# Kernel optimization log

Hardware: AMD Instinct MI355X
Metric: run time of the kernel (lower is better)

## Reference

```python
import jax, jax.numpy as jnp
import numpy as np

B, R, N, D, H, QK, K = 32, 200, 200, 128, 8, 16, 10
CLIP = 10.0  # standard POMO logit clipping


def setup_inputs() -> dict:
    key = jax.random.key(0)
    ks = jax.random.split(key, 12)
    encoded_nodes = jax.random.normal(ks[0], (B, N, D), jnp.float32)
    distance = jax.random.uniform(ks[1], (B, N, N), jnp.float32)
    current = jax.random.randint(ks[2], (B, R), 0, N)
    u = jax.random.uniform(ks[3], (B, R, N))
    ninf_mask = jnp.where(u < 0.3, -jnp.inf, 0.0).astype(jnp.float32)
    s = 0.02
    Wq = jax.random.normal(ks[4], (2 * D, H * QK), jnp.float32) * s
    Wk = jax.random.normal(ks[5], (D, H * QK), jnp.float32) * s
    Wv = jax.random.normal(ks[6], (D, H * QK), jnp.float32) * s
    Wmhc = jax.random.normal(ks[7], (H * QK, D), jnp.float32) * s
    b_mhc = jnp.zeros((D,), jnp.float32)
    W1 = jax.random.normal(ks[8], (K * D, 5 * D), jnp.float32) * s
    b1 = jnp.zeros((5 * D,), jnp.float32)
    W2 = jax.random.normal(ks[9], (5 * D, D), jnp.float32) * s
    b2 = jnp.zeros((D,), jnp.float32)
    return {"encoded_nodes": encoded_nodes, "distance": distance, "ninf_mask": ninf_mask,
            "current": current, "Wq": Wq, "Wk": Wk, "Wv": Wv, "Wmhc": Wmhc, "b_mhc": b_mhc,
            "W1": W1, "b1": b1, "W2": W2, "b2": b2}


def _search_unvisited(current, distance, ninf_mask):
    # rows of distance at current nodes: [B,R,N] (avoids B*R*N*N materialization)
    dist_f = jnp.take_along_axis(distance, current[:, :, None], axis=1)
    dist_m = jnp.where(jnp.isfinite(ninf_mask), dist_f, jnp.inf)
    neg_vals, idx = jax.lax.top_k(-dist_m, K)  # k smallest distances
    vals = -neg_vals
    return jnp.where(jnp.isinf(vals), N, idx)  # pad index N for masked-out slots


def _gather_pad0(encoded_nodes, idx):
    padded = jnp.concatenate([encoded_nodes, jnp.zeros((B, 1, D), encoded_nodes.dtype)], axis=1)
    g = jnp.take_along_axis(padded, idx.reshape(B, R * K)[:, :, None], axis=1)
    return g.reshape(B, R, K, D)


def _gather_pad_avg(a):
    # replace all-zero (pad) rows by the mean of non-zero rows within each [K,D] group
    is_zero = jnp.sum(a, axis=-1) == 0  # [B,R,K]
    cnt = jnp.maximum(jnp.sum(~is_zero, axis=-1).astype(a.dtype), 1e-9)  # [B,R]
    mean = jnp.sum(a, axis=2) / cnt[..., None]  # [B,R,D]
    return jnp.where(is_zero[..., None], mean[:, :, None, :], a)


def reference(encoded_nodes, distance, ninf_mask, current,
              Wq, Wk, Wv, Wmhc, b_mhc, W1, b1, W2, b2):
    knn = _search_unvisited(current, distance, ninf_mask)         # [B,R,K]
    a = _gather_pad0(encoded_nodes, knn)                          # [B,R,K,D]
    b = _gather_pad_avg(a)                                        # [B,R,K,D]
    h = jnp.maximum(b.reshape(B, R, K * D) @ W1 + b1, 0.0)
    unv = h @ W2 + b2                                             # [B,R,D]
    cur_emb = jnp.take_along_axis(encoded_nodes, current[:, :, None], axis=1)  # [B,R,D]
    qin = jnp.concatenate([cur_emb, unv], axis=-1)                # [B,R,2D]
    q = (qin @ Wq).reshape(B, R, H, QK).transpose(0, 2, 1, 3)     # [B,H,R,QK]
    k = (encoded_nodes @ Wk).reshape(B, N, H, QK).transpose(0, 2, 1, 3)
    v = (encoded_nodes @ Wv).reshape(B, N, H, QK).transpose(0, 2, 1, 3)
    score = jnp.einsum('bhrd,bhnd->bhrn', q, k) / jnp.sqrt(jnp.float32(QK))
    score = score + ninf_mask[:, None]                            # [B,H,R,N]
    w = jax.nn.softmax(score, axis=-1)
    out = jnp.einsum('bhrn,bhnd->bhrd', w, v)
    out = out.transpose(0, 2, 1, 3).reshape(B, R, H * QK)
    mh = out @ Wmhc + b_mhc                                       # [B,R,D]
    sh = jnp.einsum('brd,bnd->brn', mh, encoded_nodes) / jnp.sqrt(jnp.float32(D))
    logits = CLIP * jnp.tanh(sh) + ninf_mask
    return jax.nn.softmax(logits, axis=-1)                        # [B,R,N]
```

## Files before the change

kernel.cpp:

```cpp
#include <hip/hip_runtime.h>
#include <hip/hip_bf16.h>
#include <math.h>

#define Bc 32
#define Rc 200
#define Nc 200
#define Dc 128
#define Hc 8
#define QKc 16
#define Kc 10
#define BRc (Bc*Rc)

typedef __attribute__((ext_vector_type(8))) short short8;
typedef __attribute__((ext_vector_type(4))) float f32x4;
typedef unsigned long long u64;

#define GLOAD_LDS16(g, l) __builtin_amdgcn_global_load_lds( \
    (const __attribute__((address_space(1))) void*)(g), \
    (__attribute__((address_space(3))) void*)(l), 16, 0, 0)

__device__ inline void transpose_tile(const float* __restrict__ src, int lds_,
                                      __hip_bfloat16* __restrict__ dst, int ldd,
                                      int k0, int n0, float scale)
{
    __shared__ float tile[32][33];
    int tx = threadIdx.x & 31, ty = threadIdx.x >> 5;
    #pragma unroll
    for (int i = ty; i < 32; i += 8)
        tile[i][tx] = src[(size_t)(k0 + i) * lds_ + n0 + tx];
    __syncthreads();
    #pragma unroll
    for (int i = ty; i < 32; i += 8)
        dst[(size_t)(n0 + i) * ldd + k0 + tx] = __float2bfloat16(tile[tx][i] * scale);
}

__global__ __launch_bounds__(256) void prep_knn_kernel(
    const float* __restrict__ W1, const float* __restrict__ W2,
    const float* __restrict__ Wq, const float* __restrict__ Wmhc,
    const float* __restrict__ Wk, const float* __restrict__ Wv,
    const float* __restrict__ b2, const float* __restrict__ enc,
    const float* __restrict__ dist, const float* __restrict__ mask,
    const int* __restrict__ cur,
    __hip_bfloat16* __restrict__ W1t, __hip_bfloat16* __restrict__ Wkvt,
    __hip_bfloat16* __restrict__ Wmb, __hip_bfloat16* __restrict__ Wcat,
    float* __restrict__ bq, __hip_bfloat16* __restrict__ encb,
    unsigned* __restrict__ aoff, __hip_bfloat16* __restrict__ hq,
    u64* __restrict__ maskbits)
{
    int bid = blockIdx.x;
    int t = threadIdx.x;
    if (bid < 800) {
        transpose_tile(W1, 640, W1t, 1280, (bid % 40) * 32, (bid / 40) * 32, 1.f);
    } else if (bid < 816) {
        int id = bid - 800;
        transpose_tile(Wk, 128, Wkvt, 128, (id & 3) * 32, (id >> 2) * 32, 1.f);
    } else if (bid < 832) {
        int id = bid - 816;
        transpose_tile(Wv, 128, Wkvt + 128 * 128, 128, (id & 3) * 32, (id >> 2) * 32, 1.f);
    } else if (bid < 848) {
        int e = (bid - 832) * 1024 + t * 4;
        #pragma unroll
        for (int j = 0; j < 4; ++j) Wmb[e + j] = __float2bfloat16(Wmhc[e + j]);
    } else if (bid < 864) {
        int id = bid - 848;
        transpose_tile(Wq, 128, Wcat, 768, (id & 3) * 32, (id >> 2) * 32, 0.25f);
    } else if (bid < 904) {
        __shared__ float w2s[16 * 128];
        int j0 = (bid - 864) * 16;
        #pragma unroll
        for (int idx = t; idx < 16 * 128; idx += 256)
            w2s[idx] = W2[(size_t)j0 * 128 + idx];
        __syncthreads();
        int n = t & 127, half = t >> 7;
        float acc[8];
        #pragma unroll
        for (int jj = 0; jj < 8; ++jj) acc[jj] = 0.f;
        const float* wqp = Wq + (size_t)128 * 128 + n;
        #pragma unroll 8
        for (int k = 0; k < 128; ++k) {
            float wq = wqp[(size_t)k * 128];
            #pragma unroll
            for (int jj = 0; jj < 8; ++jj)
                acc[jj] = fmaf(w2s[(half * 8 + jj) * 128 + k], wq, acc[jj]);
        }
        #pragma unroll
        for (int jj = 0; jj < 8; ++jj)
            Wcat[(size_t)n * 768 + 128 + j0 + half * 8 + jj] =
                __float2bfloat16(acc[jj] * 0.25f);
    } else if (bid < 929) {
        size_t base = (size_t)(bid - 904) * 32768 + (size_t)t * 4;
        #pragma unroll 4
        for (int it = 0; it < 32; ++it) {
            size_t i = base + (size_t)it * 1024;
            float4 v = *(const float4*)(enc + i);
            encb[i + 0] = __float2bfloat16(v.x);
            encb[i + 1] = __float2bfloat16(v.y);
            encb[i + 2] = __float2bfloat16(v.z);
            encb[i + 3] = __float2bfloat16(v.w);
        }
    } else if (bid == 929) {
        __shared__ float red[128];
        int n = t & 127, half = t >> 7;
        float a0 = 0.f, a1 = 0.f;
        int kb = half * 64;
        #pragma unroll 8
        for (int k = 0; k < 64; k += 2) {
            a0 = fmaf(b2[kb + k],     Wq[(size_t)(128 + kb + k) * 128 + n], a0);
            a1 = fmaf(b2[kb + k + 1], Wq[(size_t)(128 + kb + k + 1) * 128 + n], a1);
        }
        if (half) red[n] = a0 + a1;
        __syncthreads();
        if (!half) bq[n] = (a0 + a1 + red[n]) * 0.25f;
    } else {
        int lane = t & 63, w = t >> 6;
        int br = (bid - 930) * 4 + w;
        int b = br / Rc;
        int c = cur[br];
        const float* drow = dist + ((size_t)b * Nc + c) * Nc;
        const float* mrow = mask + (size_t)br * Nc;

        float v[4];
        #pragma unroll
        for (int j = 0; j < 4; ++j) {
            int n = lane + 64 * j;
            bool allowed = false;
            float val = INFINITY;
            if (n < Nc) {
                float mv = mrow[n];
                if (!isinf(mv)) { val = drow[n]; allowed = true; }
            }
            v[j] = val;
            u64 wb = __ballot(allowed);
            if (lane == 0) maskbits[(size_t)br * 4 + j] = wb;
        }
        int idxs[Kc];
        unsigned myrow = 0;
        #pragma unroll
        for (int k = 0; k < Kc; ++k) {
            float bv = v[0]; int bn = lane;
            #pragma unroll
            for (int j = 1; j < 4; ++j) {
                if (v[j] < bv) { bv = v[j]; bn = lane + 64 * j; }
            }
            #pragma unroll
            for (int off = 32; off > 0; off >>= 1) {
                float ov = __shfl_xor(bv, off);
                int   on = __shfl_xor(bn, off);
                if (ov < bv || (ov == bv && on < bn)) { bv = ov; bn = on; }
            }
            bool pad = isinf(bv);
            idxs[k] = pad ? Nc : bn;
            if (lane == k) myrow = pad ? (unsigned)(Bc * Nc + br) : (unsigned)(b * Nc + bn);
            int oj = bn >> 6, ol = bn & 63;
            if (!pad && lane == ol) v[oj] = INFINITY;
        }
        if (lane < Kc) aoff[(size_t)br * 16 + lane] = myrow << 7;

        const float* erow = enc + ((size_t)b * Nc + c) * Dc;
        __hip_bfloat16* hrow = hq + (size_t)br * 768;
        hrow[lane]      = __float2bfloat16(erow[lane]);
        hrow[lane + 64] = __float2bfloat16(erow[lane + 64]);

        if (idxs[Kc - 1] == Nc) {
            float cnt = 0.f;
            #pragma unroll
            for (int k = 0; k < Kc; ++k) cnt += (idxs[k] < Nc) ? 1.f : 0.f;
            float icnt = 1.f / fmaxf(cnt, 1e-9f);
            #pragma unroll
            for (int half = 0; half < 2; ++half) {
                int d = lane + 64 * half;
                float sum = 0.f;
                #pragma unroll
                for (int k = 0; k < Kc; ++k) {
                    if (idxs[k] < Nc)
                        sum += enc[((size_t)b * Nc + idxs[k]) * Dc + d];
                }
                encb[((size_t)(Bc * Nc) + br) * Dc + d] = __float2bfloat16(sum * icnt);
            }
        }
    }
}

__global__ __launch_bounds__(256) void fused_gemms_kernel(
    const __hip_bfloat16* __restrict__ encb, const unsigned* __restrict__ aoff,
    const __hip_bfloat16* __restrict__ W1t, const float* __restrict__ b1,
    const __hip_bfloat16* __restrict__ Wkvt, const __hip_bfloat16* __restrict__ Wmb,
    const float* __restrict__ bmhc, const float* __restrict__ enc,
    __hip_bfloat16* __restrict__ hq, __hip_bfloat16* __restrict__ kvf,
    __hip_bfloat16* __restrict__ em, float* __restrict__ be)
{
    __shared__ short Asl[4][64 * 32];
    __shared__ short Bsl[4][64 * 32];
    int bid = blockIdx.x;
    int tid = threadIdx.x;
    int wave = tid >> 6, lane = tid & 63;
    int lrow = lane >> 2;
    int cg   = lane & 3;
    int ss   = (lane >> 3) & 3;
    int gq   = (cg - ss) & 3;
    int wm = wave >> 1, wn = wave & 1;
    int rrow = lane & 15, quad = lane >> 4;
    int srd  = (rrow >> 1) & 3;
    int strip = (wave & 1) * 32;

    if (bid < 1000) {
        int m0 = (bid / 10) * 64, n0 = (bid % 10) * 64;
        unsigned o0[Kc], o1[Kc];
        if (wave < 2) {
            const unsigned* ap0 = aoff + (size_t)(m0 + strip + lrow) * 16;
            const unsigned* ap1 = ap0 + 16 * 16;
            #pragma unroll
            for (int j = 0; j < Kc; ++j) { o0[j] = ap0[j]; o1[j] = ap1[j]; }
        }
        const short* Eb = (const short*)encb;
        const short* gB0 = (const short*)W1t + (size_t)(n0 + strip + lrow) * 1280 + gq * 8;
        const short* gB1 = gB0 + (size_t)16 * 1280;

        f32x4 acc[2][2];
        #pragma unroll
        for (int i = 0; i < 2; ++i)
            #pragma unroll
            for (int j = 0; j < 2; ++j)
                acc[i][j] = (f32x4){0.f, 0.f, 0.f, 0.f};

        #pragma unroll
        for (int kt = 0; kt < 10; ++kt) {
            __syncthreads();
            #pragma unroll
            for (int s = 0; s < 4; ++s) {
                if (wave < 2) {
                    GLOAD_LDS16(Eb + o0[kt] + s * 32 + gq * 8, &Asl[s][strip * 32]);
                    GLOAD_LDS16(Eb + o1[kt] + s * 32 + gq * 8, &Asl[s][(strip + 16) * 32]);
                } else {
                    GLOAD_LDS16(gB0 + kt * 128 + s * 32, &Bsl[s][strip * 32]);
                    GLOAD_LDS16(gB1 + kt * 128 + s * 32, &Bsl[s][(strip + 16) * 32]);
                }
            }
            __syncthreads();
            #pragma unroll
            for (int s = 0; s < 4; ++s) {
                short8 afr[2], bfr[2];
                #pragma unroll
                for (int mt = 0; mt < 2; ++mt)
                    afr[mt] = *(const short8*)&Asl[s][(wm * 32 + mt * 16 + rrow) * 32 + ((quad + srd) & 3) * 8];
                #pragma unroll
                for (int nt = 0; nt < 2; ++nt)
                    bfr[nt] = *(const short8*)&Bsl[s][(wn * 32 + nt * 16 + rrow) * 32 + ((quad + srd) & 3) * 8];
                #pragma unroll
                for (int mt = 0; mt < 2; ++mt)
                    #pragma unroll
                    for (int nt = 0; nt < 2; ++nt)
                        acc[mt][nt] = __builtin_amdgcn_mfma_f32_16x16x32_bf16(
                            afr[mt], bfr[nt], acc[mt][nt], 0, 0, 0);
            }
        }
        #pragma unroll
        for (int mt = 0; mt < 2; ++mt)
            #pragma unroll
            for (int nt = 0; nt < 2; ++nt) {
                int n = wn * 32 + nt * 16 + rrow;
                float bv = b1[n0 + n];
                #pragma unroll
                for (int i = 0; i < 4; ++i) {
                    int m = m0 + wm * 32 + mt * 16 + quad * 4 + i;
                    float vv = fmaxf(acc[mt][nt][i] + bv, 0.f);
                    hq[(size_t)m * 768 + 128 + n0 + n] = __float2bfloat16(vv);
                }
            }
    } else if (bid < 1600) {
        const short* Bbase; __hip_bfloat16* Cout; int ldc, m0, n0;
        if (bid < 1400) {
            int id = bid - 1000;
            Bbase = (const short*)Wkvt; Cout = kvf; ldc = 256;
            m0 = (id >> 2) * 64; n0 = (id & 3) * 64;
        } else {
            int id = bid - 1400;
            Bbase = (const short*)Wmb; Cout = em; ldc = 128;
            m0 = (id >> 1) * 64; n0 = (id & 1) * 64;
        }
        const short* g0 = (wave < 2)
            ? (const short*)encb + (size_t)(m0 + strip + lrow) * 128 + gq * 8
            : Bbase + (size_t)(n0 + strip + lrow) * 128 + gq * 8;
        const short* g1 = g0 + (size_t)16 * 128;

        f32x4 acc[2][2];
        #pragma unroll
        for (int i = 0; i < 2; ++i)
            #pragma unroll
            for (int j = 0; j < 2; ++j)
                acc[i][j] = (f32x4){0.f, 0.f, 0.f, 0.f};

        #pragma unroll
        for (int s = 0; s < 4; ++s) {
            short* l0 = (wave < 2) ? &Asl[s][strip * 32] : &Bsl[s][strip * 32];
            short* l1 = (wave < 2) ? &Asl[s][(strip + 16) * 32] : &Bsl[s][(strip + 16) * 32];
            GLOAD_LDS16(g0 + s * 32, l0);
            GLOAD_LDS16(g1 + s * 32, l1);
        }
        __syncthreads();
        #pragma unroll
        for (int s = 0; s < 4; ++s) {
            short8 afr[2], bfr[2];
            #pragma unroll
            for (int mt = 0; mt < 2; ++mt)
                afr[mt] = *(const short8*)&Asl[s][(wm * 32 + mt * 16 + rrow) * 32 + ((quad + srd) & 3) * 8];
            #pragma unroll
            for (int nt = 0; nt < 2; ++nt)
                bfr[nt] = *(const short8*)&Bsl[s][(wn * 32 + nt * 16 + rrow) * 32 + ((quad + srd) & 3) * 8];
            #pragma unroll
            for (int mt = 0; mt < 2; ++mt)
                #pragma unroll
                for (int nt = 0; nt < 2; ++nt)
                    acc[mt][nt] = __builtin_amdgcn_mfma_f32_16x16x32_bf16(
                        afr[mt], bfr[nt], acc[mt][nt], 0, 0, 0);
        }
        #pragma unroll
        for (int mt = 0; mt < 2; ++mt)
            #pragma unroll
            for (int nt = 0; nt < 2; ++nt) {
                int n = wn * 32 + nt * 16 + rrow;
                #pragma unroll
                for (int i = 0; i < 4; ++i) {
                    int m = m0 + wm * 32 + mt * 16 + quad * 4 + i;
                    Cout[(size_t)m * ldc + n0 + n] = __float2bfloat16(acc[mt][nt][i]);
                }
            }
    } else {
        int i = (bid - 1600) * 256 + tid;
        if (i < Bc * Nc) {
            const float* row = enc + (size_t)i * 128;
            float acc = 0.f;
            #pragma unroll
            for (int dq = 0; dq < 32; ++dq) {
                float4 e4 = *(const float4*)(row + dq * 4);
                acc = fmaf(bmhc[dq * 4 + 0], e4.x, acc);
                acc = fmaf(bmhc[dq * 4 + 1], e4.y, acc);
                acc = fmaf(bmhc[dq * 4 + 2], e4.z, acc);
                acc = fmaf(bmhc[dq * 4 + 3], e4.w, acc);
            }
            be[i] = acc;
        }
    }
}

__global__ __launch_bounds__(256) void qgemm_kernel(
    const __hip_bfloat16* __restrict__ hq, const __hip_bfloat16* __restrict__ Wcat,
    const float* __restrict__ bq, __hip_bfloat16* __restrict__ q)
{
    __shared__ short Asl[4][64 * 32];
    __shared__ short Bsl[4][64 * 32];
    int tid = threadIdx.x;
    int wave = tid >> 6, lane = tid & 63;
    int m0 = blockIdx.y * 64, n0 = blockIdx.x * 64;
    int lrow = lane >> 2;
    int cg   = lane & 3;
    int ss   = (lane >> 3) & 3;
    int gq   = (cg - ss) & 3;
    int wm = wave >> 1, wn = wave & 1;
    int rrow = lane & 15, quad = lane >> 4;
    int srd  = (rrow >> 1) & 3;
    int strip = (wave & 1) * 32;

    const short* g0 = (wave < 2)
        ? (const short*)hq + (size_t)(m0 + strip + lrow) * 768 + gq * 8
        : (const short*)Wcat + (size_t)(n0 + strip + lrow) * 768 + gq * 8;
    const short* g1 = g0 + (size_t)16 * 768;

    f32x4 acc[2][2];
    #pragma unroll
    for (int i = 0; i < 2; ++i)
        #pragma unroll
        for (int j = 0; j < 2; ++j)
            acc[i][j] = (f32x4){0.f, 0.f, 0.f, 0.f};

    for (int k0 = 0; k0 < 768; k0 += 128) {
        __syncthreads();
        #pragma unroll
        for (int s = 0; s < 4; ++s) {
            short* l0 = (wave < 2) ? &Asl[s][strip * 32] : &Bsl[s][strip * 32];
            short* l1 = (wave < 2) ? &Asl[s][(strip + 16) * 32] : &Bsl[s][(strip + 16) * 32];
            GLOAD_LDS16(g0 + k0 + s * 32, l0);
            GLOAD_LDS16(g1 + k0 + s * 32, l1);
        }
        __syncthreads();
        #pragma unroll
        for (int s = 0; s < 4; ++s) {
            short8 afr[2], bfr[2];
            #pragma unroll
            for (int mt = 0; mt < 2; ++mt)
                afr[mt] = *(const short8*)&Asl[s][(wm * 32 + mt * 16 + rrow) * 32 + ((quad + srd) & 3) * 8];
            #pragma unroll
            for (int nt = 0; nt < 2; ++nt)
                bfr[nt] = *(const short8*)&Bsl[s][(wn * 32 + nt * 16 + rrow) * 32 + ((quad + srd) & 3) * 8];
            #pragma unroll
            for (int mt = 0; mt < 2; ++mt)
                #pragma unroll
                for (int nt = 0; nt < 2; ++nt)
                    acc[mt][nt] = __builtin_amdgcn_mfma_f32_16x16x32_bf16(
                        afr[mt], bfr[nt], acc[mt][nt], 0, 0, 0);
        }
    }

    #pragma unroll
    for (int mt = 0; mt < 2; ++mt) {
        #pragma unroll
        for (int nt = 0; nt < 2; ++nt) {
            int n = wn * 32 + nt * 16 + rrow;
            float bv = bq[n0 + n];
            #pragma unroll
            for (int i = 0; i < 4; ++i) {
                int m = m0 + wm * 32 + mt * 16 + quad * 4 + i;
                q[(size_t)m * 128 + n0 + n] = __float2bfloat16(acc[mt][nt][i] + bv);
            }
        }
    }
}

__global__ __launch_bounds__(256) void attn_mfma_kernel(
    const __hip_bfloat16* __restrict__ q, const __hip_bfloat16* __restrict__ kvf,
    const u64* __restrict__ maskbits, __hip_bfloat16* __restrict__ att)
{
    constexpr int RP = 208;
    constexpr int QS = 40;
    constexpr int VS = 232;
    __shared__ short Qs[RP * QS];
    __shared__ short Ks[RP * QS];
    __shared__ short Vt[16 * VS];
    __shared__ short Ps[4][16 * VS];
    __shared__ u64 smask[RP][4];

    int b = blockIdx.x >> 3, h = blockIdx.x & 7;
    int half = blockIdx.y;
    int t = threadIdx.x;
    int wave = t >> 6, lane = t & 63;
    int rrow = lane & 15, quad = lane >> 4;

    const short8 z8 = {0, 0, 0, 0, 0, 0, 0, 0};
    for (int idx = t; idx < RP * 2; idx += 256) {
        int r = idx >> 1, g = idx & 1;
        short8 qa = z8, ka = z8;
        if (r < Rc) {
            qa = *(const short8*)((const short*)q + ((size_t)(b * Rc + r)) * 128 + h * 16 + g * 8);
            ka = *(const short8*)((const short*)kvf + ((size_t)(b * Nc + r)) * 256 + h * 16 + g * 8);
        }
        *(short8*)&Qs[r * QS + g * 8] = qa;
        *(short8*)&Ks[r * QS + g * 8] = ka;
        *(short8*)&Qs[r * QS + 16 + g * 8] = z8;
        *(short8*)&Ks[r * QS + 16 + g * 8] = z8;
    }
    if (t < Rc) {
        const short* vp = (const short*)kvf + ((size_t)(b * Nc + t)) * 256 + 128 + h * 16;
        short8 v0 = *(const short8*)vp;
        short8 v1 = *(const short8*)(vp + 8);
        #pragma unroll
        for (int d = 0; d < 8; ++d) Vt[d * VS + t] = v0[d];
        #pragma unroll
        for (int d = 0; d < 8; ++d) Vt[(d + 8) * VS + t] = v1[d];
    }
    for (int idx = t; idx < 16 * 32; idx += 256) {
        int d = idx >> 5, cN = 200 + (idx & 31);
        if (cN < VS) Vt[d * VS + cN] = 0;
    }
    for (int idx = lane; idx < 16 * 16; idx += 64) {
        int rr = idx >> 4, cc = 208 + (idx & 15);
        Ps[wave][rr * VS + cc] = 0;
    }
    for (int idx = t; idx < RP * 4; idx += 256) {
        int r = idx >> 2, w = idx & 3;
        smask[r][w] = (r < Rc) ? maskbits[((size_t)b * Rc + r) * 4 + w] : ~0ull;
    }
    __syncthreads();

    int rt0 = half * 7, rt1 = half ? 13 : 7;
    for (int rt = rt0 + wave; rt < rt1; rt += 4) {
        short8 qf = *(const short8*)&Qs[(rt * 16 + rrow) * QS + quad * 8];
        f32x4 sacc[13];
        #pragma unroll
        for (int nt = 0; nt < 13; ++nt) {
            short8 kf = *(const short8*)&Ks[(nt * 16 + rrow) * QS + quad * 8];
            sacc[nt] = __builtin_amdgcn_mfma_f32_16x16x32_bf16(
                qf, kf, (f32x4){0.f, 0.f, 0.f, 0.f}, 0, 0, 0);
        }
        float inv[4];
        #pragma unroll
        for (int i = 0; i < 4; ++i) {
            int r = rt * 16 + quad * 4 + i;
            u64 wv0 = smask[r][0], wv1 = smask[r][1], wv2 = smask[r][2], wv3 = smask[r][3];
            float mx = -INFINITY;
            #pragma unroll
            for (int nt = 0; nt < 13; ++nt) {
                u64 w = (nt < 4) ? wv0 : (nt < 8) ? wv1 : (nt < 12) ? wv2 : wv3;
                int sh = ((nt & 3) << 4) + rrow;
                float s = ((w >> sh) & 1ull) ? sacc[nt][i] : -INFINITY;
                sacc[nt][i] = s;
                mx = fmaxf(mx, s);
            }
            mx = fmaxf(mx, __shfl_xor(mx, 1));
            mx = fmaxf(mx, __shfl_xor(mx, 2));
            mx = fmaxf(mx, __shfl_xor(mx, 4));
            mx = fmaxf(mx, __shfl_xor(mx, 8));
            float l = 0.f;
            #pragma unroll
            for (int nt = 0; nt < 13; ++nt) {
                float p = __expf(sacc[nt][i] - mx);
                sacc[nt][i] = p;
                l += p;
            }
            l += __shfl_xor(l, 1);
            l += __shfl_xor(l, 2);
            l += __shfl_xor(l, 4);
            l += __shfl_xor(l, 8);
            inv[i] = (l > 0.f) ? 1.f / l : 0.f;
        }
        #pragma unroll
        for (int nt = 0; nt < 13; ++nt)
            #pragma unroll
            for (int i = 0; i < 4; ++i)
                *(__hip_bfloat16*)&Ps[wave][(quad * 4 + i) * VS + nt * 16 + rrow] =
                    __float2bfloat16(sacc[nt][i]);
        f32x4 oacc = (f32x4){0.f, 0.f, 0.f, 0.f};
        #pragma unroll
        for (int kt = 0; kt < 7; ++kt) {
            short8 pf = *(const short8*)&Ps[wave][rrow * VS + kt * 32 + quad * 8];
            short8 vf = *(const short8*)&Vt[rrow * VS + kt * 32 + quad * 8];
            oacc = __builtin_amdgcn_mfma_f32_16x16x32_bf16(pf, vf, oacc, 0, 0, 0);
        }
        #pragma unroll
        for (int i = 0; i < 4; ++i) {
            int r = rt * 16 + quad * 4 + i;
            if (r < Rc)
                att[((size_t)(b * Rc + r)) * 128 + h * 16 + rrow] =
                    __float2bfloat16(oacc[i] * inv[i]);
        }
    }
}

__global__ __launch_bounds__(256) void logits_softmax_kernel(
    const __hip_bfloat16* __restrict__ att, const __hip_bfloat16* __restrict__ em,
    const float* __restrict__ be, const u64* __restrict__ maskbits,
    float* __restrict__ out)
{
    __shared__ short Asl[4][64 * 32];
    __shared__ short Bsl[4][208 * 32];
    __shared__ u64 sm[64][4];
    __shared__ float sbe[208];
    int b = blockIdx.x, m0 = blockIdx.y * 64;
    int t = threadIdx.x, wave = t >> 6, lane = t & 63;
    int lrow = lane >> 2, cg = lane & 3, ss = (lane >> 3) & 3, gq = (cg - ss) & 3;
    int rrow = lane & 15, quad = lane >> 4, srd = (rrow >> 1) & 3;

    const short* Aa = (const short*)att + ((size_t)b * Rc + m0) * 128;
    const short* Ben = (const short*)em + (size_t)b * Nc * 128;

    #pragma unroll
    for (int kc = 0; kc < 4; ++kc)
        GLOAD_LDS16(Aa + (size_t)(wave * 16 + lrow) * 128 + kc * 32 + gq * 8,
                    &Asl[kc][(wave * 16) * 32]);
    for (int cch = wave; cch < 13; cch += 4)
        #pragma unroll
        for (int kc = 0; kc < 4; ++kc)
            GLOAD_LDS16(Ben + (size_t)(cch * 16 + lrow) * 128 + kc * 32 + gq * 8,
                        &Bsl[kc][(cch * 16) * 32]);
    {
        int r = t >> 2, w = t & 3;
        sm[r][w] = (m0 + r < Rc) ? maskbits[((size_t)b * Rc + m0 + r) * 4 + w] : 0ull;
    }
    if (t < 208) sbe[t] = (t < Nc) ? be[(size_t)b * Nc + t] : 0.f;
    __syncthreads();

    short8 afr[4];
    #pragma unroll
    for (int kc = 0; kc < 4; ++kc)
        afr[kc] = *(const short8*)&Asl[kc][(wave * 16 + rrow) * 32 + ((quad + srd) & 3) * 8];

    f32x4 acc[13];
    #pragma unroll
    for (int nt = 0; nt < 13; ++nt)
        acc[nt] = (f32x4){0.f, 0.f, 0.f, 0.f};
    #pragma unroll
    for (int nt = 0; nt < 13; ++nt)
        #pragma unroll
        for (int kc = 0; kc < 4; ++kc) {
            short8 bfr = *(const short8*)
                &Bsl[kc][(nt * 16 + rrow) * 32 + ((quad + srd) & 3) * 8];
            acc[nt] = __builtin_amdgcn_mfma_f32_16x16x32_bf16(afr[kc], bfr, acc[nt], 0, 0, 0);
        }

    const float scale = 0.08838834764831843f;
    #pragma unroll
    for (int i = 0; i < 4; ++i) {
        int rloc = wave * 16 + quad * 4 + i;
        int r = m0 + rloc;
        u64 w0 = sm[rloc][0], w1 = sm[rloc][1], w2 = sm[rloc][2], w3 = sm[rloc][3];
        float vals[13];
        float mx = -INFINITY;
        #pragma unroll
        for (int nt = 0; nt < 13; ++nt) {
            u64 w = (nt < 4) ? w0 : (nt < 8) ? w1 : (nt < 12) ? w2 : w3;
            int sh = ((nt & 3) << 4) + rrow;
            float lg = -INFINITY;
            if ((w >> sh) & 1ull) {
                float y = (acc[nt][i] + sbe[nt * 16 + rrow]) * scale;
                float e = __expf(2.f * y);
                lg = 10.f * (1.f - 2.f / (e + 1.f));
            }
            vals[nt] = lg;
            mx = fmaxf(mx, lg);
        }
        mx = fmaxf(mx, __shfl_xor(mx, 1));
        mx = fmaxf(mx, __shfl_xor(mx, 2));
        mx = fmaxf(mx, __shfl_xor(mx, 4));
        mx = fmaxf(mx, __shfl_xor(mx, 8));
        float l = 0.f;
        #pragma unroll
        for (int nt = 0; nt < 13; ++nt) {
            float p = (vals[nt] == -INFINITY) ? 0.f : __expf(vals[nt] - mx);
            vals[nt] = p;
            l += p;
        }
        l += __shfl_xor(l, 1);
        l += __shfl_xor(l, 2);
        l += __shfl_xor(l, 4);
        l += __shfl_xor(l, 8);
        float inv = (l > 0.f) ? 1.f / l : 0.f;
        if (r < Rc) {
            #pragma unroll
            for (int nt = 0; nt < 13; ++nt) {
                int n = nt * 16 + rrow;
                if (n < Nc)
                    out[((size_t)b * Rc + r) * Nc + n] = vals[nt] * inv;
            }
        }
    }
}

extern "C" void kernel_launch(void* const* d_in, const int* in_sizes, int n_in,
                              void* d_out, int out_size, void* d_ws, size_t ws_size,
                              hipStream_t stream)
{
    const float* enc  = (const float*)d_in[0];
    const float* dist = (const float*)d_in[1];
    const float* mask = (const float*)d_in[2];
    const int*   cur  = (const int*)d_in[3];
    const float* Wq   = (const float*)d_in[4];
    const float* Wk   = (const float*)d_in[5];
    const float* Wv   = (const float*)d_in[6];
    const float* Wmhc = (const float*)d_in[7];
    const float* bmhc = (const float*)d_in[8];
    const float* W1   = (const float*)d_in[9];
    const float* b1   = (const float*)d_in[10];
    const float* W2   = (const float*)d_in[11];
    const float* b2   = (const float*)d_in[12];
    float* out = (float*)d_out;

    char* ws = (char*)d_ws;
    size_t off = 0;
    auto alloc = [&](size_t bytes) { char* p = ws + off; off += (bytes + 255) & ~(size_t)255; return p; };
    __hip_bfloat16* W1t  = (__hip_bfloat16*)alloc((size_t)640 * 1280 * 2);
    __hip_bfloat16* Wkvt = (__hip_bfloat16*)alloc((size_t)256 * 128 * 2);
    __hip_bfloat16* Wmb  = (__hip_bfloat16*)alloc((size_t)128 * 128 * 2);
    __hip_bfloat16* Wcat = (__hip_bfloat16*)alloc((size_t)128 * 768 * 2);
    float* bq = (float*)alloc((size_t)128 * 4);
    __hip_bfloat16* encb = (__hip_bfloat16*)alloc((size_t)(Bc * Nc + BRc + 64) * Dc * 2);
    unsigned* aoff = (unsigned*)alloc((size_t)BRc * 16 * 4);
    __hip_bfloat16* hq   = (__hip_bfloat16*)alloc((size_t)BRc * 768 * 2);
    __hip_bfloat16* q    = (__hip_bfloat16*)alloc((size_t)BRc * 128 * 2);
    __hip_bfloat16* kvf  = (__hip_bfloat16*)alloc((size_t)Bc * Nc * 256 * 2);
    __hip_bfloat16* att  = (__hip_bfloat16*)alloc((size_t)(BRc + 64) * 128 * 2);
    __hip_bfloat16* em   = (__hip_bfloat16*)alloc((size_t)(Bc * Nc + 64) * 128 * 2);
    float* be = (float*)alloc((size_t)Bc * Nc * 4);
    u64* maskbits = (u64*)alloc((size_t)BRc * 4 * 8);

    prep_knn_kernel<<<2530, 256, 0, stream>>>(
        W1, W2, Wq, Wmhc, Wk, Wv, b2, enc, dist, mask, cur,
        W1t, Wkvt, Wmb, Wcat, bq, encb, aoff, hq, maskbits);
    fused_gemms_kernel<<<1625, 256, 0, stream>>>(
        encb, aoff, W1t, b1, Wkvt, Wmb, bmhc, enc, hq, kvf, em, be);
    qgemm_kernel<<<dim3(2, BRc / 64), 256, 0, stream>>>(hq, Wcat, bq, q);
    attn_mfma_kernel<<<dim3(Bc * Hc, 2), 256, 0, stream>>>(q, kvf, maskbits, att);
    logits_softmax_kernel<<<dim3(Bc, 4), 256, 0, stream>>>(att, em, be, maskbits, out);
}
```

Measured before the change: 162.3 us.

## Double-buffer LDS staging in W1 and Q projection GEMM loops

Two GEMM main loops, the gathered W1 layer and the Q projection, change from load-sync-compute with a 128-wide K step to a ping-pong scheme. The existing 4-slot LDS array is split into two 2-slot buffers with a 64-wide K step, and the next chunk's global-to-LDS loads are issued before computing on the current one. This removes one barrier per iteration and is meant to overlap memory latency with MFMA work. In exchange the K loop runs twice as many iterations, each with half the work.

```diff
diff --git a/kernel.cpp b/kernel.cpp
--- a/kernel.cpp
+++ b/kernel.cpp
@@ -223,37 +223,55 @@
             for (int j = 0; j < 2; ++j)
                 acc[i][j] = (f32x4){0.f, 0.f, 0.f, 0.f};
 
-        #pragma unroll
-        for (int kt = 0; kt < 10; ++kt) {
+#define G1_STAGE(bsel, kt) do {                                                   \
+            int g_ = (kt) >> 1, hh_ = ((kt) & 1) * 64;                            \
+            _Pragma("unroll")                                                     \
+            for (int s_ = 0; s_ < 2; ++s_) {                                      \
+                if (wave < 2) {                                                   \
+                    GLOAD_LDS16(Eb + o0[g_] + hh_ + s_ * 32 + gq * 8,             \
+                                &Asl[((bsel) << 1) | s_][strip * 32]);            \
+                    GLOAD_LDS16(Eb + o1[g_] + hh_ + s_ * 32 + gq * 8,             \
+                                &Asl[((bsel) << 1) | s_][(strip + 16) * 32]);     \
+                } else {                                                          \
+                    GLOAD_LDS16(gB0 + (kt) * 64 + s_ * 32,                        \
+                                &Bsl[((bsel) << 1) | s_][strip * 32]);            \
+                    GLOAD_LDS16(gB1 + (kt) * 64 + s_ * 32,                        \
+                                &Bsl[((bsel) << 1) | s_][(strip + 16) * 32]);     \
+                }                                                                 \
+            } } while (0)
+
+#define G1_COMPUTE(bsel) do {                                                     \
+            _Pragma("unroll")                                                     \
+            for (int s_ = 0; s_ < 2; ++s_) {                                      \
+                short8 afr[2], bfr[2];                                            \
+                _Pragma("unroll")                                                 \
+                for (int mt = 0; mt < 2; ++mt)                                    \
+                    afr[mt] = *(const short8*)&Asl[((bsel) << 1) | s_]            \
+                        [(wm * 32 + mt * 16 + rrow) * 32 + ((quad + srd) & 3) * 8]; \
+                _Pragma("unroll")                                                 \
+                for (int nt = 0; nt < 2; ++nt)                                    \
+                    bfr[nt] = *(const short8*)&Bsl[((bsel) << 1) | s_]            \
+                        [(wn * 32 + nt * 16 + rrow) * 32 + ((quad + srd) & 3) * 8]; \
+                _Pragma("unroll")                                                 \
+                for (int mt = 0; mt < 2; ++mt)                                    \
+                    _Pragma("unroll")                                             \
+                    for (int nt = 0; nt < 2; ++nt)                                \
+                        acc[mt][nt] = __builtin_amdgcn_mfma_f32_16x16x32_bf16(    \
+                            afr[mt], bfr[nt], acc[mt][nt], 0, 0, 0);              \
+            } } while (0)
+
+        G1_STAGE(0, 0);
+        __syncthreads();
+        #pragma unroll
+        for (int kt = 0; kt < 19; ++kt) {
+            G1_STAGE((kt & 1) ^ 1, kt + 1);
+            G1_COMPUTE(kt & 1);
             __syncthreads();
-            #pragma unroll
-            for (int s = 0; s < 4; ++s) {
-                if (wave < 2) {
-                    GLOAD_LDS16(Eb + o0[kt] + s * 32 + gq * 8, &Asl[s][strip * 32]);
-                    GLOAD_LDS16(Eb + o1[kt] + s * 32 + gq * 8, &Asl[s][(strip + 16) * 32]);
-                } else {
-                    GLOAD_LDS16(gB0 + kt * 128 + s * 32, &Bsl[s][strip * 32]);
-                    GLOAD_LDS16(gB1 + kt * 128 + s * 32, &Bsl[s][(strip + 16) * 32]);
-                }
-            }
-            __syncthreads();
-            #pragma unroll
-            for (int s = 0; s < 4; ++s) {
-                short8 afr[2], bfr[2];
-                #pragma unroll
-                for (int mt = 0; mt < 2; ++mt)
-                    afr[mt] = *(const short8*)&Asl[s][(wm * 32 + mt * 16 + rrow) * 32 + ((quad + srd) & 3) * 8];
-                #pragma unroll
-                for (int nt = 0; nt < 2; ++nt)
-                    bfr[nt] = *(const short8*)&Bsl[s][(wn * 32 + nt * 16 + rrow) * 32 + ((quad + srd) & 3) * 8];
-                #pragma unroll
-                for (int mt = 0; mt < 2; ++mt)
-                    #pragma unroll
-                    for (int nt = 0; nt < 2; ++nt)
-                        acc[mt][nt] = __builtin_amdgcn_mfma_f32_16x16x32_bf16(
-                            afr[mt], bfr[nt], acc[mt][nt], 0, 0, 0);
-            }
-        }
+        }
+        G1_COMPUTE(1);
+#undef G1_STAGE
+#undef G1_COMPUTE
+
         #pragma unroll
         for (int mt = 0; mt < 2; ++mt)
             #pragma unroll
@@ -373,33 +391,48 @@
         for (int j = 0; j < 2; ++j)
             acc[i][j] = (f32x4){0.f, 0.f, 0.f, 0.f};
 
-    for (int k0 = 0; k0 < 768; k0 += 128) {
+#define Q_STAGE(bsel, kt) do {                                                    \
+        _Pragma("unroll")                                                         \
+        for (int s_ = 0; s_ < 2; ++s_) {                                          \
+            short* l0_ = (wave < 2) ? &Asl[((bsel) << 1) | s_][strip * 32]        \
+                                    : &Bsl[((bsel) << 1) | s_][strip * 32];       \
+            short* l1_ = (wave < 2) ? &Asl[((bsel) << 1) | s_][(strip + 16) * 32] \
+                                    : &Bsl[((bsel) << 1) | s_][(strip + 16) * 32];\
+            GLOAD_LDS16(g0 + (kt) * 64 + s_ * 32, l0_);                           \
+            GLOAD_LDS16(g1 + (kt) * 64 + s_ * 32, l1_);                           \
+        } } while (0)
+
+#define Q_COMPUTE(bsel) do {                                                      \
+        _Pragma("unroll")                                                         \
+        for (int s_ = 0; s_ < 2; ++s_) {                                          \
+            short8 afr[2], bfr[2];                                                \
+            _Pragma("unroll")                                                     \
+            for (int mt = 0; mt < 2; ++mt)                                        \
+                afr[mt] = *(const short8*)&Asl[((bsel) << 1) | s_]                \
+                    [(wm * 32 + mt * 16 + rrow) * 32 + ((quad + srd) & 3) * 8];   \
+            _Pragma("unroll")                                                     \
+            for (int nt = 0; nt < 2; ++nt)                                        \
+                bfr[nt] = *(const short8*)&Bsl[((bsel) << 1) | s_]                \
+                    [(wn * 32 + nt * 16 + rrow) * 32 + ((quad + srd) & 3) * 8];   \
+            _Pragma("unroll")                                                     \
+            for (int mt = 0; mt < 2; ++mt)                                        \
+                _Pragma("unroll")                                                 \
+                for (int nt = 0; nt < 2; ++nt)                                    \
+                    acc[mt][nt] = __builtin_amdgcn_mfma_f32_16x16x32_bf16(        \
+                        afr[mt], bfr[nt], acc[mt][nt], 0, 0, 0);                  \
+        } } while (0)
+
+    Q_STAGE(0, 0);
+    __syncthreads();
+    #pragma unroll
+    for (int kt = 0; kt < 11; ++kt) {
+        Q_STAGE((kt & 1) ^ 1, kt + 1);
+        Q_COMPUTE(kt & 1);
         __syncthreads();
-        #pragma unroll
-        for (int s = 0; s < 4; ++s) {
-            short* l0 = (wave < 2) ? &Asl[s][strip * 32] : &Bsl[s][strip * 32];
-            short* l1 = (wave < 2) ? &Asl[s][(strip + 16) * 32] : &Bsl[s][(strip + 16) * 32];
-            GLOAD_LDS16(g0 + k0 + s * 32, l0);
-            GLOAD_LDS16(g1 + k0 + s * 32, l1);
-        }
-        __syncthreads();
-        #pragma unroll
-        for (int s = 0; s < 4; ++s) {
-            short8 afr[2], bfr[2];
-            #pragma unroll
-            for (int mt = 0; mt < 2; ++mt)
-                afr[mt] = *(const short8*)&Asl[s][(wm * 32 + mt * 16 + rrow) * 32 + ((quad + srd) & 3) * 8];
-            #pragma unroll
-            for (int nt = 0; nt < 2; ++nt)
-                bfr[nt] = *(const short8*)&Bsl[s][(wn * 32 + nt * 16 + rrow) * 32 + ((quad + srd) & 3) * 8];
-            #pragma unroll
-            for (int mt = 0; mt < 2; ++mt)
-                #pragma unroll
-                for (int nt = 0; nt < 2; ++nt)
-                    acc[mt][nt] = __builtin_amdgcn_mfma_f32_16x16x32_bf16(
-                        afr[mt], bfr[nt], acc[mt][nt], 0, 0, 0);
-        }
-    }
+    }
+    Q_COMPUTE(1);
+#undef Q_STAGE
+#undef Q_COMPUTE
 
     #pragma unroll
     for (int mt = 0; mt < 2; ++mt) {
```

After: 161.2 us. Within noise of the previous version (-0.7%).
